# Optimization experiments

Measured on AMD Instinct MI355X. Metric: run time of the kernel, lower is better.

## Reference

```python
import jax, jax.numpy as jnp
import numpy as np

N_BINS = 10


def setup_inputs() -> dict:
    key = jax.random.key(0)
    k1, k2 = jax.random.split(key)
    N, C = 1000000, 128
    logits = jax.random.normal(k1, (N, C), dtype=jnp.float32)
    labels = jax.random.randint(k2, (N,), 0, C, dtype=jnp.int64)
    return {"logits": logits, "labels": labels}


def reference(logits, labels):
    N = logits.shape[0]
    probs = jax.nn.softmax(logits, axis=1)
    confidences = jnp.max(probs, axis=1)          # [N]
    predictions = jnp.argmax(probs, axis=1)       # [N]
    accuracies = (predictions == labels).astype(jnp.float32)

    # Bin i covers (i/n, (i+1)/n]; ceil(conf*n)-1 gives that index.
    bin_idx = jnp.clip(
        jnp.ceil(confidences * N_BINS).astype(jnp.int32) - 1, 0, N_BINS - 1
    )

    counts = jax.ops.segment_sum(jnp.ones_like(confidences), bin_idx, num_segments=N_BINS)
    conf_sum = jax.ops.segment_sum(confidences, bin_idx, num_segments=N_BINS)
    acc_sum = jax.ops.segment_sum(accuracies, bin_idx, num_segments=N_BINS)

    prop_in_bin = counts / N
    nonempty = counts > 0
    denom = jnp.maximum(counts, 1.0)
    acc_in_bin = jnp.where(nonempty, acc_sum / denom, 0.0)
    conf_in_bin = jnp.where(nonempty, conf_sum / denom, 0.0)

    CE = conf_in_bin - acc_in_bin
    abs_CE = jnp.where(nonempty, jnp.abs(CE), 0.0)
    ece = jnp.sum(abs_CE * prop_in_bin)
    oe = jnp.sum(jnp.where(nonempty, conf_in_bin * jnp.maximum(CE, 0.0), 0.0) * prop_in_bin)

    # (ece, per-bin accuracy, oe, per-bin proportion, per-bin |CE|)
    return ece, acc_in_bin, oe, prop_in_bin, abs_CE
```

## Files before the change

kernel.cpp:

```cpp
#include <hip/hip_runtime.h>

#define N_BINS 10

template<int CTRL, bool BC>
__device__ __forceinline__ float dpp_f(float x, float old_) {
    int r = __builtin_amdgcn_update_dpp(__builtin_bit_cast(int, old_),
                                        __builtin_bit_cast(int, x),
                                        CTRL, 0xf, 0xf, BC);
    return __builtin_bit_cast(float, r);
}

__device__ __forceinline__ float half_reduce_add(float x) {
    x += dpp_f<0x111, true>(x, 0.f);
    x += dpp_f<0x112, true>(x, 0.f);
    x += dpp_f<0x114, true>(x, 0.f);
    x += dpp_f<0x118, true>(x, 0.f);
    x += dpp_f<0x142, true>(x, 0.f);
    return x;
}

__device__ __forceinline__ float half_reduce_max(float x) {
    x = fmaxf(x, dpp_f<0x111, false>(x, x));
    x = fmaxf(x, dpp_f<0x112, false>(x, x));
    x = fmaxf(x, dpp_f<0x114, false>(x, x));
    x = fmaxf(x, dpp_f<0x118, false>(x, x));
    x = fmaxf(x, dpp_f<0x142, false>(x, x));
    return x;
}

__global__ void ece_zero_ws(unsigned int* ws) {
    int i = threadIdx.x;
    if (i < 64) ws[i] = 0u;
}

__global__ __launch_bounds__(256) void ece_main(
        const float* __restrict__ logits,
        const int*   __restrict__ labels,
        float*       __restrict__ ws,
        int N) {
    __shared__ float              s_conf[N_BINS];
    __shared__ unsigned long long s_pack[N_BINS];
    if (threadIdx.x < N_BINS) {
        s_conf[threadIdx.x] = 0.f;
        s_pack[threadIdx.x] = 0ull;
    }
    __syncthreads();

    const int lane32       = threadIdx.x & 31;
    const int rowInBlock   = threadIdx.x >> 5;
    const int rowsPerBlock = blockDim.x >> 5;

    long long row = (long long)blockIdx.x * rowsPerBlock + rowInBlock;
    const long long rowStride = (long long)gridDim.x * rowsPerBlock;

    for (; row < N; row += rowStride) {
        const float4* p = (const float4*)(logits + row * 128);
        float4 v = p[lane32];
        int la = labels[row];

        float m4 = fmaxf(fmaxf(v.x, v.y), fmaxf(v.z, v.w));
        float e4 = __expf(v.x) + __expf(v.y) + __expf(v.z) + __expf(v.w);
        float vl = 0.f;
        if ((la >> 2) == lane32) {
            int r = la & 3;
            vl = (r == 0) ? v.x : (r == 1) ? v.y : (r == 2) ? v.z : v.w;
        }

        float S  = half_reduce_add(e4);
        float M  = half_reduce_max(m4);
        float VL = half_reduce_add(vl);

        if (lane32 == 31) {
            float conf = __expf(M) / S;
            int bin = (int)ceilf(conf * 10.0f) - 1;
            bin = min(max(bin, 0), N_BINS - 1);
            unsigned long long packed = 0x100000000ull | (unsigned long long)(VL == M ? 1u : 0u);
            atomicAdd(&s_conf[bin], conf);
            atomicAdd(&s_pack[bin], packed);
        }
    }

    __syncthreads();
    if (threadIdx.x < N_BINS) {
        atomicAdd(&ws[threadIdx.x], s_conf[threadIdx.x]);
        atomicAdd((unsigned long long*)((char*)ws + 64) + threadIdx.x, s_pack[threadIdx.x]);
    }
}

__global__ void ece_finalize(const float* __restrict__ ws, float* __restrict__ out, int N) {
    if (threadIdx.x == 0 && blockIdx.x == 0) {
        const unsigned long long* pack = (const unsigned long long*)((const char*)ws + 64);
        float ece = 0.f, oe = 0.f;
        for (int b = 0; b < N_BINS; ++b) {
            float cs = ws[b];
            unsigned long long pk = pack[b];
            unsigned int c  = (unsigned int)(pk >> 32);
            float as        = (float)(unsigned int)(pk & 0xffffffffull);
            float cnt   = (float)c;
            float prop  = cnt / (float)N;
            float denom = fmaxf(cnt, 1.0f);
            bool  ne    = (c > 0);
            float acc_in  = ne ? as / denom : 0.f;
            float conf_in = ne ? cs / denom : 0.f;
            float CE    = conf_in - acc_in;
            float absCE = ne ? fabsf(CE) : 0.f;
            ece += absCE * prop;
            oe  += (ne ? conf_in * fmaxf(CE, 0.f) : 0.f) * prop;
            out[1 + b]  = acc_in;
            out[12 + b] = prop;
            out[22 + b] = absCE;
        }
        out[0]  = ece;
        out[11] = oe;
    }
}

extern "C" void kernel_launch(void* const* d_in, const int* in_sizes, int n_in,
                              void* d_out, int out_size, void* d_ws, size_t ws_size,
                              hipStream_t stream) {
    const float* logits = (const float*)d_in[0];
    const int*   labels = (const int*)d_in[1];
    float*       out    = (float*)d_out;
    float*       ws     = (float*)d_ws;
    const int N = in_sizes[1];

    hipLaunchKernelGGL(ece_zero_ws, dim3(1), dim3(64), 0, stream, (unsigned int*)ws);

    const int block = 256;
    const int rowsPerBlock = block / 32;
    int grid = (N + rowsPerBlock - 1) / rowsPerBlock;
    if (grid > 2048) grid = 2048;
    hipLaunchKernelGGL(ece_main, dim3(grid), dim3(block), 0, stream,
                       logits, labels, ws, N);

    hipLaunchKernelGGL(ece_finalize, dim3(1), dim3(64), 0, stream, ws, out, N);
}
```

Before: 654.6 us.

## Process four rows per half-wave with batched loads and per-slot shared bins

Result: no change. 659.7 us (+0.8%).

```diff
diff --git a/kernel.cpp b/kernel.cpp
--- a/kernel.cpp
+++ b/kernel.cpp
@@ -1,6 +1,7 @@
 #include <hip/hip_runtime.h>
 
 #define N_BINS 10
+#define SLOTS  8
 
 template<int CTRL, bool BC>
 __device__ __forceinline__ float dpp_f(float x, float old_) {
@@ -38,52 +39,67 @@
         const int*   __restrict__ labels,
         float*       __restrict__ ws,
         int N) {
-    __shared__ float              s_conf[N_BINS];
-    __shared__ unsigned long long s_pack[N_BINS];
-    if (threadIdx.x < N_BINS) {
-        s_conf[threadIdx.x] = 0.f;
-        s_pack[threadIdx.x] = 0ull;
+    __shared__ float              s_conf[SLOTS][N_BINS];
+    __shared__ unsigned long long s_pack[SLOTS][N_BINS];
+    if (threadIdx.x < SLOTS * N_BINS) {
+        ((float*)s_conf)[threadIdx.x]              = 0.f;
+        ((unsigned long long*)s_pack)[threadIdx.x] = 0ull;
     }
     __syncthreads();
 
-    const int lane32       = threadIdx.x & 31;
-    const int rowInBlock   = threadIdx.x >> 5;
-    const int rowsPerBlock = blockDim.x >> 5;
+    const int lane32 = threadIdx.x & 31;
+    const int hw     = threadIdx.x >> 5;
 
-    long long row = (long long)blockIdx.x * rowsPerBlock + rowInBlock;
-    const long long rowStride = (long long)gridDim.x * rowsPerBlock;
+    long long base = ((long long)blockIdx.x * SLOTS + hw) * 4;
+    const long long stride = (long long)gridDim.x * SLOTS * 4;
 
-    for (; row < N; row += rowStride) {
-        const float4* p = (const float4*)(logits + row * 128);
-        float4 v = p[lane32];
-        int la = labels[row];
+    for (; base < N; base += stride) {
+        const float4* p = (const float4*)(logits + base * 128);
+        float4 v0 = p[0 * 32 + lane32];
+        float4 v1 = p[1 * 32 + lane32];
+        float4 v2 = p[2 * 32 + lane32];
+        float4 v3 = p[3 * 32 + lane32];
+        int4 lab = *(const int4*)(labels + base);
 
-        float m4 = fmaxf(fmaxf(v.x, v.y), fmaxf(v.z, v.w));
-        float e4 = __expf(v.x) + __expf(v.y) + __expf(v.z) + __expf(v.w);
-        float vl = 0.f;
-        if ((la >> 2) == lane32) {
-            int r = la & 3;
-            vl = (r == 0) ? v.x : (r == 1) ? v.y : (r == 2) ? v.z : v.w;
-        }
+        #pragma unroll
+        for (int k = 0; k < 4; ++k) {
+            float4 v = (k == 0) ? v0 : (k == 1) ? v1 : (k == 2) ? v2 : v3;
+            int    la = (k == 0) ? lab.x : (k == 1) ? lab.y : (k == 2) ? lab.z : lab.w;
 
-        float S  = half_reduce_add(e4);
-        float M  = half_reduce_max(m4);
-        float VL = half_reduce_add(vl);
+            float m4 = fmaxf(fmaxf(v.x, v.y), fmaxf(v.z, v.w));
+            float e4 = __expf(v.x) + __expf(v.y) + __expf(v.z) + __expf(v.w);
+            float vl = 0.f;
+            if ((la >> 2) == lane32) {
+                int r = la & 3;
+                vl = (r == 0) ? v.x : (r == 1) ? v.y : (r == 2) ? v.z : v.w;
+            }
 
-        if (lane32 == 31) {
-            float conf = __expf(M) / S;
-            int bin = (int)ceilf(conf * 10.0f) - 1;
-            bin = min(max(bin, 0), N_BINS - 1);
-            unsigned long long packed = 0x100000000ull | (unsigned long long)(VL == M ? 1u : 0u);
-            atomicAdd(&s_conf[bin], conf);
-            atomicAdd(&s_pack[bin], packed);
+            float S  = half_reduce_add(e4);
+            float M  = half_reduce_max(m4);
+            float VL = half_reduce_add(vl);
+
+            if (lane32 == 31) {
+                float conf = __expf(M) / S;
+                int bin = (int)ceilf(conf * 10.0f) - 1;
+                bin = min(max(bin, 0), N_BINS - 1);
+                unsigned long long packed =
+                    0x100000000ull | (unsigned long long)(VL == M ? 1u : 0u);
+                atomicAdd(&s_conf[hw][bin], conf);
+                atomicAdd(&s_pack[hw][bin], packed);
+            }
         }
     }
 
     __syncthreads();
     if (threadIdx.x < N_BINS) {
-        atomicAdd(&ws[threadIdx.x], s_conf[threadIdx.x]);
-        atomicAdd((unsigned long long*)((char*)ws + 64) + threadIdx.x, s_pack[threadIdx.x]);
+        float cf = 0.f; unsigned long long pk = 0ull;
+        #pragma unroll
+        for (int s = 0; s < SLOTS; ++s) {
+            cf += s_conf[s][threadIdx.x];
+            pk += s_pack[s][threadIdx.x];
+        }
+        atomicAdd(&ws[threadIdx.x], cf);
+        atomicAdd((unsigned long long*)((char*)ws + 64) + threadIdx.x, pk);
     }
 }
 
@@ -126,11 +142,8 @@
 
     hipLaunchKernelGGL(ece_zero_ws, dim3(1), dim3(64), 0, stream, (unsigned int*)ws);
 
-    const int block = 256;
-    const int rowsPerBlock = block / 32;
-    int grid = (N + rowsPerBlock - 1) / rowsPerBlock;
-    if (grid > 2048) grid = 2048;
-    hipLaunchKernelGGL(ece_main, dim3(grid), dim3(block), 0, stream,
+    const int grid = 1024;
+    hipLaunchKernelGGL(ece_main, dim3(grid), dim3(256), 0, stream,
                        logits, labels, ws, N);
 
     hipLaunchKernelGGL(ece_finalize, dim3(1), dim3(64), 0, stream, ws, out, N);
```
